# Kernel optimization log

Hardware: AMD Instinct MI355X
Metric: run time of the kernel (lower is better)

Reference implementation:

```python
import jax, jax.numpy as jnp
import numpy as np

N_NODES = 20000
N_EDGES = 320000
NUM_GRAPHS = 64
IN_DIM = 256


def setup_inputs() -> dict:
    key = jax.random.key(0)
    ks = jax.random.split(key, 12)
    x = jax.random.normal(ks[0], (N_NODES, IN_DIM), dtype=jnp.float32)
    edge_index = jax.random.randint(ks[1], (2, N_EDGES), 0, N_NODES, dtype=jnp.int64)
    batch = jnp.sort(jax.random.randint(ks[2], (N_NODES,), 0, NUM_GRAPHS, dtype=jnp.int64))
    def glorot(k, shape):
        lim = float(np.sqrt(6.0 / (shape[0] + shape[1])))
        return jax.random.uniform(k, shape, dtype=jnp.float32, minval=-lim, maxval=lim)
    W1 = glorot(ks[3], (IN_DIM, 256)); b1 = jnp.zeros((256,), jnp.float32)
    W2 = glorot(ks[4], (256, 128));   b2 = jnp.zeros((128,), jnp.float32)
    Wl1 = glorot(ks[5], (128, 64));   bl1 = jnp.zeros((64,), jnp.float32)
    Wl2 = glorot(ks[6], (64, 1));     bl2 = jnp.zeros((1,), jnp.float32)
    return {"x": x, "edge_index": edge_index, "batch": batch,
            "W1": W1, "b1": b1, "W2": W2, "b2": b2,
            "Wl1": Wl1, "bl1": bl1, "Wl2": Wl2, "bl2": bl2}


def gcn_conv(x, src, dst, W, b, n_nodes):
    # PyG GCNConv: add self-loops, symmetric normalization D^-1/2 (A+I) D^-1/2,
    # linear transform first, then gather-scale-scatter aggregation, then bias.
    loop = jnp.arange(n_nodes, dtype=src.dtype)
    s = jnp.concatenate([src, loop])
    d = jnp.concatenate([dst, loop])
    deg = jax.ops.segment_sum(jnp.ones_like(d, dtype=x.dtype), d, num_segments=n_nodes)
    dinv = jnp.where(deg > 0, jax.lax.rsqrt(deg), 0.0)
    norm = dinv[s] * dinv[d]                         # [E+N]
    h = x @ W                                        # [N, out]
    msg = h[s] * norm[:, None]                       # [E+N, out]
    out = jax.ops.segment_sum(msg, d, num_segments=n_nodes)
    return out + b


def global_mean_pool(x, batch, num_graphs):
    sums = jax.ops.segment_sum(x, batch, num_segments=num_graphs)
    cnts = jax.ops.segment_sum(jnp.ones((x.shape[0],), x.dtype), batch, num_segments=num_graphs)
    return sums / jnp.maximum(cnts, 1.0)[:, None]


def reference(x, edge_index, batch, W1, b1, W2, b2, Wl1, bl1, Wl2, bl2):
    n = x.shape[0]
    src, dst = edge_index[0], edge_index[1]
    h = jax.nn.relu(gcn_conv(x, src, dst, W1, b1, n))   # dropout = identity (eval)
    h = jax.nn.relu(gcn_conv(h, src, dst, W2, b2, n))
    g = global_mean_pool(h, batch, NUM_GRAPHS)          # [G, 128]
    g = jax.nn.relu(g @ Wl1 + bl1)
    return jax.nn.sigmoid(g @ Wl2 + bl2)                # [G, 1]
```

## Files before the change

kernel.cpp:

```cpp
#include <hip/hip_runtime.h>
#include <hip/hip_bf16.h>
#include <math.h>

typedef __attribute__((ext_vector_type(8))) short bf16x8;
typedef __attribute__((ext_vector_type(4))) float f32x4;

__device__ __forceinline__ unsigned short f2bf(float f) {
    unsigned int u = __float_as_uint(f);
    unsigned int r = (u + 0x7FFFu + ((u >> 16) & 1u)) >> 16;
    return (unsigned short)r;
}
__device__ __forceinline__ float bf2f(unsigned short h) {
    return __uint_as_float(((unsigned int)h) << 16);
}
__device__ __forceinline__ float bfe(short s) {
    return __uint_as_float(((unsigned int)(unsigned short)s) << 16);
}
__device__ __forceinline__ unsigned char f2fp8(float v) {
    int p = __builtin_amdgcn_cvt_pk_fp8_f32(v, v, 0, false);
    return (unsigned char)(p & 0xff);
}
__device__ __forceinline__ unsigned int pk4fp8(float a, float b, float c, float d) {
    int p = __builtin_amdgcn_cvt_pk_fp8_f32(a, b, 0, false);
    p = __builtin_amdgcn_cvt_pk_fp8_f32(c, d, p, true);
    return (unsigned int)p;
}
__device__ __forceinline__ void fp8x8_fma(uint2 u, float w, float* a) {
    a[0] += __builtin_amdgcn_cvt_f32_fp8((int)u.x, 0) * w;
    a[1] += __builtin_amdgcn_cvt_f32_fp8((int)u.x, 1) * w;
    a[2] += __builtin_amdgcn_cvt_f32_fp8((int)u.x, 2) * w;
    a[3] += __builtin_amdgcn_cvt_f32_fp8((int)u.x, 3) * w;
    a[4] += __builtin_amdgcn_cvt_f32_fp8((int)u.y, 0) * w;
    a[5] += __builtin_amdgcn_cvt_f32_fp8((int)u.y, 1) * w;
    a[6] += __builtin_amdgcn_cvt_f32_fp8((int)u.y, 2) * w;
    a[7] += __builtin_amdgcn_cvt_f32_fp8((int)u.y, 3) * w;
}
__device__ __forceinline__ void fp8x4_fma(unsigned int u, float w, float* a) {
    a[0] += __builtin_amdgcn_cvt_f32_fp8((int)u, 0) * w;
    a[1] += __builtin_amdgcn_cvt_f32_fp8((int)u, 1) * w;
    a[2] += __builtin_amdgcn_cvt_f32_fp8((int)u, 2) * w;
    a[3] += __builtin_amdgcn_cvt_f32_fp8((int)u, 3) * w;
}
__device__ __forceinline__ float deg_dinv(int c) { return rsqrtf((float)c + 1.0f); }

__device__ __forceinline__ void load_lds16(const unsigned short* g, unsigned short* l) {
    __builtin_amdgcn_global_load_lds(
        (const __attribute__((address_space(1))) unsigned int*)g,
        (__attribute__((address_space(3))) unsigned int*)l, 16, 0, 0);
}

__global__ __launch_bounds__(256) void prep_kernel(const int* __restrict__ src,
                                                   const int* __restrict__ dst,
                                                   int* __restrict__ cnt,
                                                   int* __restrict__ csr,
                                                   const float* __restrict__ x,
                                                   unsigned short* __restrict__ xh,
                                                   const int* __restrict__ batch,
                                                   int* __restrict__ gstart,
                                                   const float* __restrict__ W1,
                                                   unsigned short* __restrict__ w1th,
                                                   unsigned short* __restrict__ w1tl,
                                                   const float* __restrict__ W2,
                                                   unsigned short* __restrict__ w2th,
                                                   unsigned short* __restrict__ w2tl,
                                                   int N, int E, int G,
                                                   int FB, int CXB, int BNB) {
    int b = blockIdx.x;
    int tid = threadIdx.x;
    if (b < FB) {
        int e = b * 256 + tid;
        if (e < E) {
            int d = dst[e];
            int slot = atomicAdd(&cnt[d], 1);
            if (slot < 64) csr[(d << 6) + slot] = src[e];
        }
        return;
    }
    b -= FB;
    if (b < CXB) {
        size_t idx = (size_t)b * 256 + tid;
        size_t total4 = (size_t)N * 64;
        if (idx < total4) {
            float4 v = ((const float4*)x)[idx];
            ushort4 o;
            o.x = f2bf(v.x); o.y = f2bf(v.y); o.z = f2bf(v.z); o.w = f2bf(v.w);
            ((ushort4*)xh)[idx] = o;
        }
        return;
    }
    b -= CXB;
    if (b < BNB) {
        int i = b * 256 + tid;
        if (i >= N) return;
        int bb = batch[i];
        if (i == 0) { for (int g = 0; g <= bb; g++) gstart[g] = 0; }
        else { int bp = batch[i - 1]; for (int g = bp + 1; g <= bb; g++) gstart[g] = i; }
        if (i == N - 1) { for (int g = bb + 1; g <= G; g++) gstart[g] = N; }
        return;
    }
    b -= BNB;
    {
        int idx = b * 256 + tid;
        if (idx < 256 * 256) {
            int m = idx >> 8, k = idx & 255;
            float w = W1[(size_t)k * 256 + m];
            unsigned short hi = f2bf(w);
            w1th[idx] = hi;
            w1tl[idx] = f2bf(w - bf2f(hi));
        } else if (idx < 256 * 256 + 128 * 256) {
            int j = idx - 256 * 256;
            int m = j >> 8, k = j & 255;
            float w = W2[(size_t)k * 128 + m];
            unsigned short hi = f2bf(w);
            w2th[j] = hi;
            w2tl[j] = f2bf(w - bf2f(hi));
        }
    }
}

__global__ __launch_bounds__(256) void gemm_kernel(const unsigned short* __restrict__ A,
                                                   const unsigned short* __restrict__ Bth,
                                                   const unsigned short* __restrict__ Btl,
                                                   unsigned char* __restrict__ C8,
                                                   int N, int M) {
    __shared__ unsigned short As[128 * 32];
    __shared__ unsigned short Bhs[64 * 32];
    __shared__ unsigned short Bls[64 * 32];
    const int K = 256;
    int tid = threadIdx.x;
    int wave = tid >> 6, lane = tid & 63;
    int quad = lane >> 4, m16 = lane & 15;
    int r0 = blockIdx.y * 128, c0 = blockIdx.x * 64;
    int srow = lane >> 2;
    int skoff = (lane & 3) * 8;

    f32x4 acc[2][4];
#pragma unroll
    for (int rg = 0; rg < 2; rg++)
#pragma unroll
        for (int ct = 0; ct < 4; ct++) acc[rg][ct] = (f32x4){0.f, 0.f, 0.f, 0.f};

    for (int kb = 0; kb < K; kb += 32) {
#pragma unroll
        for (int i = 0; i < 2; i++) {
            int brow = wave * 32 + i * 16 + srow;
            int grow = r0 + brow; if (grow >= N) grow = N - 1;
            load_lds16(A + (size_t)grow * K + kb + skoff, As + (wave * 32 + i * 16) * 32);
        }
        {
            int bcol = wave * 16 + srow;
            size_t goff = (size_t)(c0 + bcol) * K + kb + skoff;
            load_lds16(Bth + goff, Bhs + (wave * 16) * 32);
            load_lds16(Btl + goff, Bls + (wave * 16) * 32);
        }
        __syncthreads();
        bf16x8 af[2], bh[4], bl[4];
#pragma unroll
        for (int rg = 0; rg < 2; rg++)
            af[rg] = *(const bf16x8*)(As + (wave * 32 + rg * 16 + m16) * 32 + quad * 8);
#pragma unroll
        for (int ct = 0; ct < 4; ct++) {
            bh[ct] = *(const bf16x8*)(Bhs + (ct * 16 + m16) * 32 + quad * 8);
            bl[ct] = *(const bf16x8*)(Bls + (ct * 16 + m16) * 32 + quad * 8);
        }
#pragma unroll
        for (int rg = 0; rg < 2; rg++)
#pragma unroll
            for (int ct = 0; ct < 4; ct++) {
                acc[rg][ct] = __builtin_amdgcn_mfma_f32_16x16x32_bf16(af[rg], bh[ct], acc[rg][ct], 0, 0, 0);
                acc[rg][ct] = __builtin_amdgcn_mfma_f32_16x16x32_bf16(af[rg], bl[ct], acc[rg][ct], 0, 0, 0);
            }
        __syncthreads();
    }
#pragma unroll
    for (int rg = 0; rg < 2; rg++) {
#pragma unroll
        for (int ct = 0; ct < 4; ct++) {
            int col = c0 + ct * 16 + m16;
#pragma unroll
            for (int r = 0; r < 4; r++) {
                int row = r0 + wave * 32 + rg * 16 + quad * 4 + r;
                if (row < N) C8[(size_t)row * M + col] = f2fp8(acc[rg][ct][r]);
            }
        }
    }
}

__global__ __launch_bounds__(256) void gather256_kernel(const unsigned char* __restrict__ h8,
                                                        const int* __restrict__ csr,
                                                        const int* __restrict__ cnt,
                                                        const float* __restrict__ bias,
                                                        unsigned short* __restrict__ out, int N) {
    int node = blockIdx.x * 4 + (threadIdx.x >> 6);
    if (node >= N) return;
    int lane = threadIdx.x & 63;
    int half = lane >> 5, hl = lane & 31;
    int beg = node << 6;
    int c = cnt[node]; if (c > 64) c = 64;
    int end = beg + c;
    float a[8] = {0, 0, 0, 0, 0, 0, 0, 0};
    int j = beg;
    for (; j + 7 < end; j += 8) {
        int s0 = csr[j + half], s1 = csr[j + 2 + half];
        int s2 = csr[j + 4 + half], s3 = csr[j + 6 + half];
        float w0 = deg_dinv(cnt[s0]), w1 = deg_dinv(cnt[s1]);
        float w2 = deg_dinv(cnt[s2]), w3 = deg_dinv(cnt[s3]);
        uint2 u0 = *(const uint2*)(h8 + (size_t)s0 * 256 + hl * 8);
        uint2 u1 = *(const uint2*)(h8 + (size_t)s1 * 256 + hl * 8);
        uint2 u2 = *(const uint2*)(h8 + (size_t)s2 * 256 + hl * 8);
        uint2 u3 = *(const uint2*)(h8 + (size_t)s3 * 256 + hl * 8);
        fp8x8_fma(u0, w0, a); fp8x8_fma(u1, w1, a);
        fp8x8_fma(u2, w2, a); fp8x8_fma(u3, w3, a);
    }
    for (; j + 1 < end; j += 2) {
        int s0 = csr[j + half];
        float w0 = deg_dinv(cnt[s0]);
        uint2 u0 = *(const uint2*)(h8 + (size_t)s0 * 256 + hl * 8);
        fp8x8_fma(u0, w0, a);
    }
    if (j < end && half == 0) {
        int s0 = csr[j];
        float w0 = deg_dinv(cnt[s0]);
        uint2 u0 = *(const uint2*)(h8 + (size_t)s0 * 256 + hl * 8);
        fp8x8_fma(u0, w0, a);
    }
#pragma unroll
    for (int i = 0; i < 8; i++) a[i] += __shfl_down(a[i], 32);
    if (half == 0) {
        float dd = deg_dinv(c);
        float self[8] = {0, 0, 0, 0, 0, 0, 0, 0};
        uint2 uh = *(const uint2*)(h8 + (size_t)node * 256 + hl * 8);
        fp8x8_fma(uh, dd, self);
        float4 bv0 = ((const float4*)bias)[hl * 2];
        float4 bv1 = ((const float4*)bias)[hl * 2 + 1];
        float bvf[8] = {bv0.x, bv0.y, bv0.z, bv0.w, bv1.x, bv1.y, bv1.z, bv1.w};
        bf16x8 o;
#pragma unroll
        for (int i = 0; i < 8; i++)
            o[i] = (short)f2bf(fmaxf((a[i] + self[i]) * dd + bvf[i], 0.f));
        ((bf16x8*)(out + (size_t)node * 256))[hl] = o;
    }
}

__global__ __launch_bounds__(256) void gather128_kernel(const unsigned char* __restrict__ t8,
                                                        const int* __restrict__ csr,
                                                        const int* __restrict__ cnt,
                                                        const float* __restrict__ bias,
                                                        unsigned char* __restrict__ out2, int N) {
    int node = blockIdx.x * 4 + (threadIdx.x >> 6);
    if (node >= N) return;
    int lane = threadIdx.x & 63;
    int half = lane >> 5, hl = lane & 31;
    int beg = node << 6;
    int c = cnt[node]; if (c > 64) c = 64;
    int end = beg + c;
    float a[4] = {0, 0, 0, 0};
    int j = beg;
    for (; j + 7 < end; j += 8) {
        int s0 = csr[j + half], s1 = csr[j + 2 + half];
        int s2 = csr[j + 4 + half], s3 = csr[j + 6 + half];
        float w0 = deg_dinv(cnt[s0]), w1 = deg_dinv(cnt[s1]);
        float w2 = deg_dinv(cnt[s2]), w3 = deg_dinv(cnt[s3]);
        unsigned int u0 = *(const unsigned int*)(t8 + (size_t)s0 * 128 + hl * 4);
        unsigned int u1 = *(const unsigned int*)(t8 + (size_t)s1 * 128 + hl * 4);
        unsigned int u2 = *(const unsigned int*)(t8 + (size_t)s2 * 128 + hl * 4);
        unsigned int u3 = *(const unsigned int*)(t8 + (size_t)s3 * 128 + hl * 4);
        fp8x4_fma(u0, w0, a); fp8x4_fma(u1, w1, a);
        fp8x4_fma(u2, w2, a); fp8x4_fma(u3, w3, a);
    }
    for (; j + 1 < end; j += 2) {
        int s0 = csr[j + half];
        float w0 = deg_dinv(cnt[s0]);
        unsigned int u0 = *(const unsigned int*)(t8 + (size_t)s0 * 128 + hl * 4);
        fp8x4_fma(u0, w0, a);
    }
    if (j < end && half == 0) {
        int s0 = csr[j];
        float w0 = deg_dinv(cnt[s0]);
        unsigned int u0 = *(const unsigned int*)(t8 + (size_t)s0 * 128 + hl * 4);
        fp8x4_fma(u0, w0, a);
    }
#pragma unroll
    for (int i = 0; i < 4; i++) a[i] += __shfl_down(a[i], 32);
    if (half == 0) {
        float dd = deg_dinv(c);
        float self[4] = {0, 0, 0, 0};
        unsigned int uh = *(const unsigned int*)(t8 + (size_t)node * 128 + hl * 4);
        fp8x4_fma(uh, dd, self);
        float4 bv = ((const float4*)bias)[hl];
        float r0 = fmaxf((a[0] + self[0]) * dd + bv.x, 0.f);
        float r1 = fmaxf((a[1] + self[1]) * dd + bv.y, 0.f);
        float r2 = fmaxf((a[2] + self[2]) * dd + bv.z, 0.f);
        float r3 = fmaxf((a[3] + self[3]) * dd + bv.w, 0.f);
        ((unsigned int*)(out2 + (size_t)node * 128))[hl] = pk4fp8(r0, r1, r2, r3);
    }
}

__global__ __launch_bounds__(256) void poolhead_kernel(const unsigned char* __restrict__ out2,
                                                       const int* __restrict__ gstart,
                                                       const float* __restrict__ Wl1,
                                                       const float* __restrict__ bl1,
                                                       const float* __restrict__ Wl2,
                                                       const float* __restrict__ bl2,
                                                       float* __restrict__ out) {
    int g = blockIdx.x;
    int tid = threadIdx.x;
    int hw = tid >> 5, hl = tid & 31;
    int gs = gstart[g], ge = gstart[g + 1];
    float a[4] = {0, 0, 0, 0};
    int i = gs + hw;
    for (; i + 8 < ge; i += 16) {
        unsigned int u0 = ((const unsigned int*)(out2 + (size_t)i * 128))[hl];
        unsigned int u1 = ((const unsigned int*)(out2 + (size_t)(i + 8) * 128))[hl];
        fp8x4_fma(u0, 1.0f, a);
        fp8x4_fma(u1, 1.0f, a);
    }
    if (i < ge) {
        unsigned int u0 = ((const unsigned int*)(out2 + (size_t)i * 128))[hl];
        fp8x4_fma(u0, 1.0f, a);
    }
    __shared__ float red[8][128];
#pragma unroll
    for (int k = 0; k < 4; k++) red[hw][hl * 4 + k] = a[k];
    __syncthreads();
    __shared__ float gv[128];
    if (tid < 128) {
        float s = 0.f;
#pragma unroll
        for (int w = 0; w < 8; w++) s += red[w][tid];
        float cntf = fmaxf((float)(ge - gs), 1.0f);
        gv[tid] = s / cntf;
    }
    __syncthreads();
    if (tid < 64) {
        float acc = bl1[tid];
#pragma unroll 8
        for (int k = 0; k < 128; k++) acc += gv[k] * Wl1[k * 64 + tid];
        acc = fmaxf(acc, 0.f);
        float p = acc * Wl2[tid];
#pragma unroll
        for (int off = 32; off; off >>= 1) p += __shfl_down(p, off);
        if (tid == 0) out[g] = 1.f / (1.f + expf(-(p + bl2[0])));
    }
}

extern "C" void kernel_launch(void* const* d_in, const int* in_sizes, int n_in,
                              void* d_out, int out_size, void* d_ws, size_t ws_size,
                              hipStream_t stream) {
    const float* x   = (const float*)d_in[0];
    const int* ei    = (const int*)d_in[1];
    const int* batch = (const int*)d_in[2];
    const float* W1  = (const float*)d_in[3];
    const float* b1  = (const float*)d_in[4];
    const float* W2  = (const float*)d_in[5];
    const float* b2  = (const float*)d_in[6];
    const float* Wl1 = (const float*)d_in[7];
    const float* bl1 = (const float*)d_in[8];
    const float* Wl2 = (const float*)d_in[9];
    const float* bl2 = (const float*)d_in[10];
    float* out = (float*)d_out;

    const int N = in_sizes[2];
    const int E = in_sizes[1] / 2;
    const int G = 64;
    const int* src = ei;
    const int* dst = ei + E;

    char* base = (char*)d_ws;
    size_t off = 0;
    auto carve = [&](size_t bytes) -> char* {
        char* p = base + off;
        off = (off + bytes + 15) & ~(size_t)15;
        return p;
    };
    int*   cnt    = (int*)carve((size_t)N * 4);
    int*   csr    = (int*)carve((size_t)N * 64 * 4);
    int*   gstart = (int*)carve((size_t)(G + 1) * 4);
    unsigned short* w1th = (unsigned short*)carve((size_t)256 * 256 * 2);
    unsigned short* w1tl = (unsigned short*)carve((size_t)256 * 256 * 2);
    unsigned short* w2th = (unsigned short*)carve((size_t)128 * 256 * 2);
    unsigned short* w2tl = (unsigned short*)carve((size_t)128 * 256 * 2);
    unsigned short* xh   = (unsigned short*)carve((size_t)N * 256 * 2);
    unsigned char*  h8   = (unsigned char*)carve((size_t)N * 256);
    unsigned short* o1h  = (unsigned short*)carve((size_t)N * 256 * 2);
    unsigned char* t8   = (unsigned char*)xh;
    unsigned char* out2 = h8;

    hipMemsetAsync(cnt, 0, (size_t)N * 4, stream);

    const int FB  = (E + 255) / 256;
    const int CXB = (int)(((size_t)N * 64 + 255) / 256);
    const int BNB = (N + 255) / 256;
    const int CWB = (256 * 256 + 128 * 256 + 255) / 256;
    prep_kernel<<<FB + CXB + BNB + CWB, 256, 0, stream>>>(
        src, dst, cnt, csr, x, xh, batch, gstart, W1, w1th, w1tl, W2, w2th, w2tl,
        N, E, G, FB, CXB, BNB);

    {
        dim3 grid(4, (N + 127) / 128);
        gemm_kernel<<<grid, 256, 0, stream>>>(xh, w1th, w1tl, h8, N, 256);
    }
    gather256_kernel<<<(N + 3) / 4, 256, 0, stream>>>(h8, csr, cnt, b1, o1h, N);

    {
        dim3 grid(2, (N + 127) / 128);
        gemm_kernel<<<grid, 256, 0, stream>>>(o1h, w2th, w2tl, t8, N, 128);
    }
    gather128_kernel<<<(N + 3) / 4, 256, 0, stream>>>(t8, csr, cnt, b2, out2, N);

    poolhead_kernel<<<G, 256, 0, stream>>>(out2, gstart, Wl1, bl1, Wl2, bl2, out);
}
```

Baseline: 175.4 us.

## Fuse all stages into one cooperative persistent kernel with grid syncs

Replaces the memset plus six separate kernel launches with a single cooperative persistent kernel. Stages are separated by grid-wide barriers, and each stage's work is distributed over a grid-stride loop. The CSR edge fill now runs concurrently with the first GEMM tiles, since the GEMM does not depend on it. The aim is to remove launch overhead and inter-kernel gaps, at the cost of grid.sync latency and a persistent grid sized from occupancy (capped at 2048 blocks), which may lower per-stage parallelism.

```diff
diff --git a/kernel.cpp b/kernel.cpp
--- a/kernel.cpp
+++ b/kernel.cpp
@@ -1,6 +1,9 @@
 #include <hip/hip_runtime.h>
 #include <hip/hip_bf16.h>
+#include <hip/hip_cooperative_groups.h>
 #include <math.h>
+
+namespace cg = cooperative_groups;
 
 typedef __attribute__((ext_vector_type(8))) short bf16x8;
 typedef __attribute__((ext_vector_type(4))) float f32x4;
@@ -12,9 +15,6 @@
 }
 __device__ __forceinline__ float bf2f(unsigned short h) {
     return __uint_as_float(((unsigned int)h) << 16);
-}
-__device__ __forceinline__ float bfe(short s) {
-    return __uint_as_float(((unsigned int)(unsigned short)s) << 16);
 }
 __device__ __forceinline__ unsigned char f2fp8(float v) {
     int p = __builtin_amdgcn_cvt_pk_fp8_f32(v, v, 0, false);
@@ -49,7 +49,74 @@
         (__attribute__((address_space(3))) unsigned int*)l, 16, 0, 0);
 }
 
-__global__ __launch_bounds__(256) void prep_kernel(const int* __restrict__ src,
+__device__ __forceinline__ void gemm_tile_body(const unsigned short* __restrict__ A,
+                                               const unsigned short* __restrict__ Bth,
+                                               const unsigned short* __restrict__ Btl,
+                                               unsigned char* __restrict__ C8,
+                                               int N, int M, int bx, int by,
+                                               unsigned short* As, unsigned short* Bhs,
+                                               unsigned short* Bls) {
+    const int K = 256;
+    int tid = threadIdx.x;
+    int wave = tid >> 6, lane = tid & 63;
+    int quad = lane >> 4, m16 = lane & 15;
+    int r0 = by * 128, c0 = bx * 64;
+    int srow = lane >> 2;
+    int skoff = (lane & 3) * 8;
+
+    f32x4 acc[2][4];
+#pragma unroll
+    for (int rg = 0; rg < 2; rg++)
+#pragma unroll
+        for (int ct = 0; ct < 4; ct++) acc[rg][ct] = (f32x4){0.f, 0.f, 0.f, 0.f};
+
+    for (int kb = 0; kb < K; kb += 32) {
+#pragma unroll
+        for (int i = 0; i < 2; i++) {
+            int brow = wave * 32 + i * 16 + srow;
+            int grow = r0 + brow; if (grow >= N) grow = N - 1;
+            load_lds16(A + (size_t)grow * K + kb + skoff, As + (wave * 32 + i * 16) * 32);
+        }
+        {
+            int bcol = wave * 16 + srow;
+            size_t goff = (size_t)(c0 + bcol) * K + kb + skoff;
+            load_lds16(Bth + goff, Bhs + (wave * 16) * 32);
+            load_lds16(Btl + goff, Bls + (wave * 16) * 32);
+        }
+        __syncthreads();
+        bf16x8 af[2], bh[4], bl[4];
+#pragma unroll
+        for (int rg = 0; rg < 2; rg++)
+            af[rg] = *(const bf16x8*)(As + (wave * 32 + rg * 16 + m16) * 32 + quad * 8);
+#pragma unroll
+        for (int ct = 0; ct < 4; ct++) {
+            bh[ct] = *(const bf16x8*)(Bhs + (ct * 16 + m16) * 32 + quad * 8);
+            bl[ct] = *(const bf16x8*)(Bls + (ct * 16 + m16) * 32 + quad * 8);
+        }
+#pragma unroll
+        for (int rg = 0; rg < 2; rg++)
+#pragma unroll
+            for (int ct = 0; ct < 4; ct++) {
+                acc[rg][ct] = __builtin_amdgcn_mfma_f32_16x16x32_bf16(af[rg], bh[ct], acc[rg][ct], 0, 0, 0);
+                acc[rg][ct] = __builtin_amdgcn_mfma_f32_16x16x32_bf16(af[rg], bl[ct], acc[rg][ct], 0, 0, 0);
+            }
+        __syncthreads();
+    }
+#pragma unroll
+    for (int rg = 0; rg < 2; rg++) {
+#pragma unroll
+        for (int ct = 0; ct < 4; ct++) {
+            int col = c0 + ct * 16 + m16;
+#pragma unroll
+            for (int r = 0; r < 4; r++) {
+                int row = r0 + wave * 32 + rg * 16 + quad * 4 + r;
+                if (row < N) C8[(size_t)row * M + col] = f2fp8(acc[rg][ct][r]);
+            }
+        }
+    }
+}
+
+__global__ __launch_bounds__(256) void mega_kernel(const int* __restrict__ src,
                                                    const int* __restrict__ dst,
                                                    int* __restrict__ cnt,
                                                    int* __restrict__ csr,
@@ -63,284 +130,256 @@
                                                    const float* __restrict__ W2,
                                                    unsigned short* __restrict__ w2th,
                                                    unsigned short* __restrict__ w2tl,
-                                                   int N, int E, int G,
-                                                   int FB, int CXB, int BNB) {
-    int b = blockIdx.x;
+                                                   const float* __restrict__ b1,
+                                                   unsigned char* __restrict__ h8,
+                                                   unsigned short* __restrict__ o1h,
+                                                   const float* __restrict__ b2,
+                                                   unsigned char* __restrict__ t8,
+                                                   unsigned char* __restrict__ out2,
+                                                   const float* __restrict__ Wl1,
+                                                   const float* __restrict__ bl1,
+                                                   const float* __restrict__ Wl2,
+                                                   const float* __restrict__ bl2,
+                                                   float* __restrict__ out,
+                                                   int N, int E, int G) {
+    __shared__ unsigned short smem[128 * 32 + 64 * 32 + 64 * 32];
+    unsigned short* As  = smem;
+    unsigned short* Bhs = smem + 128 * 32;
+    unsigned short* Bls = smem + 128 * 32 + 64 * 32;
+    cg::grid_group grid = cg::this_grid();
     int tid = threadIdx.x;
-    if (b < FB) {
-        int e = b * 256 + tid;
-        if (e < E) {
-            int d = dst[e];
-            int slot = atomicAdd(&cnt[d], 1);
-            if (slot < 64) csr[(d << 6) + slot] = src[e];
-        }
-        return;
-    }
-    b -= FB;
-    if (b < CXB) {
-        size_t idx = (size_t)b * 256 + tid;
-        size_t total4 = (size_t)N * 64;
-        if (idx < total4) {
-            float4 v = ((const float4*)x)[idx];
-            ushort4 o;
-            o.x = f2bf(v.x); o.y = f2bf(v.y); o.z = f2bf(v.z); o.w = f2bf(v.w);
-            ((ushort4*)xh)[idx] = o;
-        }
-        return;
-    }
-    b -= CXB;
-    if (b < BNB) {
-        int i = b * 256 + tid;
-        if (i >= N) return;
-        int bb = batch[i];
-        if (i == 0) { for (int g = 0; g <= bb; g++) gstart[g] = 0; }
-        else { int bp = batch[i - 1]; for (int g = bp + 1; g <= bb; g++) gstart[g] = i; }
-        if (i == N - 1) { for (int g = bb + 1; g <= G; g++) gstart[g] = N; }
-        return;
-    }
-    b -= BNB;
+    int nblk = gridDim.x;
+
     {
-        int idx = b * 256 + tid;
-        if (idx < 256 * 256) {
-            int m = idx >> 8, k = idx & 255;
-            float w = W1[(size_t)k * 256 + m];
-            unsigned short hi = f2bf(w);
-            w1th[idx] = hi;
-            w1tl[idx] = f2bf(w - bf2f(hi));
-        } else if (idx < 256 * 256 + 128 * 256) {
-            int j = idx - 256 * 256;
-            int m = j >> 8, k = j & 255;
-            float w = W2[(size_t)k * 128 + m];
-            unsigned short hi = f2bf(w);
-            w2th[j] = hi;
-            w2tl[j] = f2bf(w - bf2f(hi));
-        }
-    }
-}
-
-__global__ __launch_bounds__(256) void gemm_kernel(const unsigned short* __restrict__ A,
-                                                   const unsigned short* __restrict__ Bth,
-                                                   const unsigned short* __restrict__ Btl,
-                                                   unsigned char* __restrict__ C8,
-                                                   int N, int M) {
-    __shared__ unsigned short As[128 * 32];
-    __shared__ unsigned short Bhs[64 * 32];
-    __shared__ unsigned short Bls[64 * 32];
-    const int K = 256;
-    int tid = threadIdx.x;
-    int wave = tid >> 6, lane = tid & 63;
-    int quad = lane >> 4, m16 = lane & 15;
-    int r0 = blockIdx.y * 128, c0 = blockIdx.x * 64;
-    int srow = lane >> 2;
-    int skoff = (lane & 3) * 8;
-
-    f32x4 acc[2][4];
-#pragma unroll
-    for (int rg = 0; rg < 2; rg++)
-#pragma unroll
-        for (int ct = 0; ct < 4; ct++) acc[rg][ct] = (f32x4){0.f, 0.f, 0.f, 0.f};
-
-    for (int kb = 0; kb < K; kb += 32) {
-#pragma unroll
-        for (int i = 0; i < 2; i++) {
-            int brow = wave * 32 + i * 16 + srow;
-            int grow = r0 + brow; if (grow >= N) grow = N - 1;
-            load_lds16(A + (size_t)grow * K + kb + skoff, As + (wave * 32 + i * 16) * 32);
-        }
-        {
-            int bcol = wave * 16 + srow;
-            size_t goff = (size_t)(c0 + bcol) * K + kb + skoff;
-            load_lds16(Bth + goff, Bhs + (wave * 16) * 32);
-            load_lds16(Btl + goff, Bls + (wave * 16) * 32);
-        }
+        const int ZB  = (N + 255) >> 8;
+        const int CXB = (int)(((size_t)N * 64 + 255) >> 8);
+        const int BNB = (N + 255) >> 8;
+        const int CWB = (256 * 256 + 128 * 256 + 255) >> 8;
+        const int TOT = ZB + CXB + BNB + CWB;
+        for (int b = blockIdx.x; b < TOT; b += nblk) {
+            int bb = b;
+            if (bb < ZB) {
+                int i = bb * 256 + tid;
+                if (i < N) cnt[i] = 0;
+                continue;
+            }
+            bb -= ZB;
+            if (bb < CXB) {
+                size_t idx = (size_t)bb * 256 + tid;
+                if (idx < (size_t)N * 64) {
+                    float4 v = ((const float4*)x)[idx];
+                    ushort4 o;
+                    o.x = f2bf(v.x); o.y = f2bf(v.y); o.z = f2bf(v.z); o.w = f2bf(v.w);
+                    ((ushort4*)xh)[idx] = o;
+                }
+                continue;
+            }
+            bb -= CXB;
+            if (bb < BNB) {
+                int i = bb * 256 + tid;
+                if (i < N) {
+                    int bv = batch[i];
+                    if (i == 0) { for (int g = 0; g <= bv; g++) gstart[g] = 0; }
+                    else { int bp = batch[i - 1]; for (int g = bp + 1; g <= bv; g++) gstart[g] = i; }
+                    if (i == N - 1) { for (int g = bv + 1; g <= G; g++) gstart[g] = N; }
+                }
+                continue;
+            }
+            bb -= BNB;
+            {
+                int idx = bb * 256 + tid;
+                if (idx < 256 * 256) {
+                    int m = idx >> 8, k = idx & 255;
+                    float w = W1[(size_t)k * 256 + m];
+                    unsigned short hi = f2bf(w);
+                    w1th[idx] = hi;
+                    w1tl[idx] = f2bf(w - bf2f(hi));
+                } else if (idx < 256 * 256 + 128 * 256) {
+                    int j = idx - 256 * 256;
+                    int m = j >> 8, k = j & 255;
+                    float w = W2[(size_t)k * 128 + m];
+                    unsigned short hi = f2bf(w);
+                    w2th[j] = hi;
+                    w2tl[j] = f2bf(w - bf2f(hi));
+                }
+            }
+        }
+    }
+    grid.sync();
+
+    {
+        const int FB = (E + 255) >> 8;
+        const int T1 = (N + 127) >> 7;
+        const int TOT = FB + 4 * T1;
+        for (int b = blockIdx.x; b < TOT; b += nblk) {
+            if (b < FB) {
+                int e = b * 256 + tid;
+                if (e < E) {
+                    int d = dst[e];
+                    int slot = atomicAdd(&cnt[d], 1);
+                    if (slot < 64) csr[(d << 6) + slot] = src[e];
+                }
+            } else {
+                int gb = b - FB;
+                gemm_tile_body(xh, w1th, w1tl, h8, N, 256, gb & 3, gb >> 2, As, Bhs, Bls);
+            }
+        }
+    }
+    grid.sync();
+
+    for (int base = blockIdx.x * 4; base < N; base += nblk * 4) {
+        int node = base + (tid >> 6);
+        if (node < N) {
+            int lane = tid & 63;
+            int half = lane >> 5, hl = lane & 31;
+            int beg = node << 6;
+            int c = cnt[node]; if (c > 64) c = 64;
+            int end = beg + c;
+            float a[8] = {0, 0, 0, 0, 0, 0, 0, 0};
+            int j = beg;
+            for (; j + 7 < end; j += 8) {
+                int s0 = csr[j + half], s1 = csr[j + 2 + half];
+                int s2 = csr[j + 4 + half], s3 = csr[j + 6 + half];
+                float w0 = deg_dinv(cnt[s0]), w1 = deg_dinv(cnt[s1]);
+                float w2 = deg_dinv(cnt[s2]), w3 = deg_dinv(cnt[s3]);
+                uint2 u0 = *(const uint2*)(h8 + (size_t)s0 * 256 + hl * 8);
+                uint2 u1 = *(const uint2*)(h8 + (size_t)s1 * 256 + hl * 8);
+                uint2 u2 = *(const uint2*)(h8 + (size_t)s2 * 256 + hl * 8);
+                uint2 u3 = *(const uint2*)(h8 + (size_t)s3 * 256 + hl * 8);
+                fp8x8_fma(u0, w0, a); fp8x8_fma(u1, w1, a);
+                fp8x8_fma(u2, w2, a); fp8x8_fma(u3, w3, a);
+            }
+            for (; j + 1 < end; j += 2) {
+                int s0 = csr[j + half];
+                float w0 = deg_dinv(cnt[s0]);
+                uint2 u0 = *(const uint2*)(h8 + (size_t)s0 * 256 + hl * 8);
+                fp8x8_fma(u0, w0, a);
+            }
+            if (j < end && half == 0) {
+                int s0 = csr[j];
+                float w0 = deg_dinv(cnt[s0]);
+                uint2 u0 = *(const uint2*)(h8 + (size_t)s0 * 256 + hl * 8);
+                fp8x8_fma(u0, w0, a);
+            }
+#pragma unroll
+            for (int i = 0; i < 8; i++) a[i] += __shfl_down(a[i], 32);
+            if (half == 0) {
+                float dd = deg_dinv(c);
+                float self[8] = {0, 0, 0, 0, 0, 0, 0, 0};
+                uint2 uh = *(const uint2*)(h8 + (size_t)node * 256 + hl * 8);
+                fp8x8_fma(uh, dd, self);
+                float4 bv0 = ((const float4*)b1)[hl * 2];
+                float4 bv1 = ((const float4*)b1)[hl * 2 + 1];
+                float bvf[8] = {bv0.x, bv0.y, bv0.z, bv0.w, bv1.x, bv1.y, bv1.z, bv1.w};
+                bf16x8 o;
+#pragma unroll
+                for (int i = 0; i < 8; i++)
+                    o[i] = (short)f2bf(fmaxf((a[i] + self[i]) * dd + bvf[i], 0.f));
+                ((bf16x8*)(o1h + (size_t)node * 256))[hl] = o;
+            }
+        }
+    }
+    grid.sync();
+
+    {
+        const int T1 = (N + 127) >> 7;
+        for (int b = blockIdx.x; b < 2 * T1; b += nblk)
+            gemm_tile_body(o1h, w2th, w2tl, t8, N, 128, b & 1, b >> 1, As, Bhs, Bls);
+    }
+    grid.sync();
+
+    for (int base = blockIdx.x * 4; base < N; base += nblk * 4) {
+        int node = base + (tid >> 6);
+        if (node < N) {
+            int lane = tid & 63;
+            int half = lane >> 5, hl = lane & 31;
+            int beg = node << 6;
+            int c = cnt[node]; if (c > 64) c = 64;
+            int end = beg + c;
+            float a[4] = {0, 0, 0, 0};
+            int j = beg;
+            for (; j + 7 < end; j += 8) {
+                int s0 = csr[j + half], s1 = csr[j + 2 + half];
+                int s2 = csr[j + 4 + half], s3 = csr[j + 6 + half];
+                float w0 = deg_dinv(cnt[s0]), w1 = deg_dinv(cnt[s1]);
+                float w2 = deg_dinv(cnt[s2]), w3 = deg_dinv(cnt[s3]);
+                unsigned int u0 = *(const unsigned int*)(t8 + (size_t)s0 * 128 + hl * 4);
+                unsigned int u1 = *(const unsigned int*)(t8 + (size_t)s1 * 128 + hl * 4);
+                unsigned int u2 = *(const unsigned int*)(t8 + (size_t)s2 * 128 + hl * 4);
+                unsigned int u3 = *(const unsigned int*)(t8 + (size_t)s3 * 128 + hl * 4);
+                fp8x4_fma(u0, w0, a); fp8x4_fma(u1, w1, a);
+                fp8x4_fma(u2, w2, a); fp8x4_fma(u3, w3, a);
+            }
+            for (; j + 1 < end; j += 2) {
+                int s0 = csr[j + half];
+                float w0 = deg_dinv(cnt[s0]);
+                unsigned int u0 = *(const unsigned int*)(t8 + (size_t)s0 * 128 + hl * 4);
+                fp8x4_fma(u0, w0, a);
+            }
+            if (j < end && half == 0) {
+                int s0 = csr[j];
+                float w0 = deg_dinv(cnt[s0]);
+                unsigned int u0 = *(const unsigned int*)(t8 + (size_t)s0 * 128 + hl * 4);
+                fp8x4_fma(u0, w0, a);
+            }
+#pragma unroll
+            for (int i = 0; i < 4; i++) a[i] += __shfl_down(a[i], 32);
+            if (half == 0) {
+                float dd = deg_dinv(c);
+                float self[4] = {0, 0, 0, 0};
+                unsigned int uh = *(const unsigned int*)(t8 + (size_t)node * 128 + hl * 4);
+                fp8x4_fma(uh, dd, self);
+                float4 bv = ((const float4*)b2)[hl];
+                float r0 = fmaxf((a[0] + self[0]) * dd + bv.x, 0.f);
+                float r1 = fmaxf((a[1] + self[1]) * dd + bv.y, 0.f);
+                float r2 = fmaxf((a[2] + self[2]) * dd + bv.z, 0.f);
+                float r3 = fmaxf((a[3] + self[3]) * dd + bv.w, 0.f);
+                ((unsigned int*)(out2 + (size_t)node * 128))[hl] = pk4fp8(r0, r1, r2, r3);
+            }
+        }
+    }
+    grid.sync();
+
+    if (blockIdx.x < (unsigned)G) {
+        int g = blockIdx.x;
+        int hw = tid >> 5, hl = tid & 31;
+        int gs = gstart[g], ge = gstart[g + 1];
+        float a[4] = {0, 0, 0, 0};
+        int i = gs + hw;
+        for (; i + 8 < ge; i += 16) {
+            unsigned int u0 = ((const unsigned int*)(out2 + (size_t)i * 128))[hl];
+            unsigned int u1 = ((const unsigned int*)(out2 + (size_t)(i + 8) * 128))[hl];
+            fp8x4_fma(u0, 1.0f, a);
+            fp8x4_fma(u1, 1.0f, a);
+        }
+        if (i < ge) {
+            unsigned int u0 = ((const unsigned int*)(out2 + (size_t)i * 128))[hl];
+            fp8x4_fma(u0, 1.0f, a);
+        }
+        float* red = (float*)smem;
+        float* gv  = red + 8 * 128;
         __syncthreads();
-        bf16x8 af[2], bh[4], bl[4];
-#pragma unroll
-        for (int rg = 0; rg < 2; rg++)
-            af[rg] = *(const bf16x8*)(As + (wave * 32 + rg * 16 + m16) * 32 + quad * 8);
-#pragma unroll
-        for (int ct = 0; ct < 4; ct++) {
-            bh[ct] = *(const bf16x8*)(Bhs + (ct * 16 + m16) * 32 + quad * 8);
-            bl[ct] = *(const bf16x8*)(Bls + (ct * 16 + m16) * 32 + quad * 8);
-        }
-#pragma unroll
-        for (int rg = 0; rg < 2; rg++)
-#pragma unroll
-            for (int ct = 0; ct < 4; ct++) {
-                acc[rg][ct] = __builtin_amdgcn_mfma_f32_16x16x32_bf16(af[rg], bh[ct], acc[rg][ct], 0, 0, 0);
-                acc[rg][ct] = __builtin_amdgcn_mfma_f32_16x16x32_bf16(af[rg], bl[ct], acc[rg][ct], 0, 0, 0);
-            }
+#pragma unroll
+        for (int k = 0; k < 4; k++) red[hw * 128 + hl * 4 + k] = a[k];
         __syncthreads();
-    }
-#pragma unroll
-    for (int rg = 0; rg < 2; rg++) {
-#pragma unroll
-        for (int ct = 0; ct < 4; ct++) {
-            int col = c0 + ct * 16 + m16;
-#pragma unroll
-            for (int r = 0; r < 4; r++) {
-                int row = r0 + wave * 32 + rg * 16 + quad * 4 + r;
-                if (row < N) C8[(size_t)row * M + col] = f2fp8(acc[rg][ct][r]);
-            }
-        }
-    }
-}
-
-__global__ __launch_bounds__(256) void gather256_kernel(const unsigned char* __restrict__ h8,
-                                                        const int* __restrict__ csr,
-                                                        const int* __restrict__ cnt,
-                                                        const float* __restrict__ bias,
-                                                        unsigned short* __restrict__ out, int N) {
-    int node = blockIdx.x * 4 + (threadIdx.x >> 6);
-    if (node >= N) return;
-    int lane = threadIdx.x & 63;
-    int half = lane >> 5, hl = lane & 31;
-    int beg = node << 6;
-    int c = cnt[node]; if (c > 64) c = 64;
-    int end = beg + c;
-    float a[8] = {0, 0, 0, 0, 0, 0, 0, 0};
-    int j = beg;
-    for (; j + 7 < end; j += 8) {
-        int s0 = csr[j + half], s1 = csr[j + 2 + half];
-        int s2 = csr[j + 4 + half], s3 = csr[j + 6 + half];
-        float w0 = deg_dinv(cnt[s0]), w1 = deg_dinv(cnt[s1]);
-        float w2 = deg_dinv(cnt[s2]), w3 = deg_dinv(cnt[s3]);
-        uint2 u0 = *(const uint2*)(h8 + (size_t)s0 * 256 + hl * 8);
-        uint2 u1 = *(const uint2*)(h8 + (size_t)s1 * 256 + hl * 8);
-        uint2 u2 = *(const uint2*)(h8 + (size_t)s2 * 256 + hl * 8);
-        uint2 u3 = *(const uint2*)(h8 + (size_t)s3 * 256 + hl * 8);
-        fp8x8_fma(u0, w0, a); fp8x8_fma(u1, w1, a);
-        fp8x8_fma(u2, w2, a); fp8x8_fma(u3, w3, a);
-    }
-    for (; j + 1 < end; j += 2) {
-        int s0 = csr[j + half];
-        float w0 = deg_dinv(cnt[s0]);
-        uint2 u0 = *(const uint2*)(h8 + (size_t)s0 * 256 + hl * 8);
-        fp8x8_fma(u0, w0, a);
-    }
-    if (j < end && half == 0) {
-        int s0 = csr[j];
-        float w0 = deg_dinv(cnt[s0]);
-        uint2 u0 = *(const uint2*)(h8 + (size_t)s0 * 256 + hl * 8);
-        fp8x8_fma(u0, w0, a);
-    }
-#pragma unroll
-    for (int i = 0; i < 8; i++) a[i] += __shfl_down(a[i], 32);
-    if (half == 0) {
-        float dd = deg_dinv(c);
-        float self[8] = {0, 0, 0, 0, 0, 0, 0, 0};
-        uint2 uh = *(const uint2*)(h8 + (size_t)node * 256 + hl * 8);
-        fp8x8_fma(uh, dd, self);
-        float4 bv0 = ((const float4*)bias)[hl * 2];
-        float4 bv1 = ((const float4*)bias)[hl * 2 + 1];
-        float bvf[8] = {bv0.x, bv0.y, bv0.z, bv0.w, bv1.x, bv1.y, bv1.z, bv1.w};
-        bf16x8 o;
-#pragma unroll
-        for (int i = 0; i < 8; i++)
-            o[i] = (short)f2bf(fmaxf((a[i] + self[i]) * dd + bvf[i], 0.f));
-        ((bf16x8*)(out + (size_t)node * 256))[hl] = o;
-    }
-}
-
-__global__ __launch_bounds__(256) void gather128_kernel(const unsigned char* __restrict__ t8,
-                                                        const int* __restrict__ csr,
-                                                        const int* __restrict__ cnt,
-                                                        const float* __restrict__ bias,
-                                                        unsigned char* __restrict__ out2, int N) {
-    int node = blockIdx.x * 4 + (threadIdx.x >> 6);
-    if (node >= N) return;
-    int lane = threadIdx.x & 63;
-    int half = lane >> 5, hl = lane & 31;
-    int beg = node << 6;
-    int c = cnt[node]; if (c > 64) c = 64;
-    int end = beg + c;
-    float a[4] = {0, 0, 0, 0};
-    int j = beg;
-    for (; j + 7 < end; j += 8) {
-        int s0 = csr[j + half], s1 = csr[j + 2 + half];
-        int s2 = csr[j + 4 + half], s3 = csr[j + 6 + half];
-        float w0 = deg_dinv(cnt[s0]), w1 = deg_dinv(cnt[s1]);
-        float w2 = deg_dinv(cnt[s2]), w3 = deg_dinv(cnt[s3]);
-        unsigned int u0 = *(const unsigned int*)(t8 + (size_t)s0 * 128 + hl * 4);
-        unsigned int u1 = *(const unsigned int*)(t8 + (size_t)s1 * 128 + hl * 4);
-        unsigned int u2 = *(const unsigned int*)(t8 + (size_t)s2 * 128 + hl * 4);
-        unsigned int u3 = *(const unsigned int*)(t8 + (size_t)s3 * 128 + hl * 4);
-        fp8x4_fma(u0, w0, a); fp8x4_fma(u1, w1, a);
-        fp8x4_fma(u2, w2, a); fp8x4_fma(u3, w3, a);
-    }
-    for (; j + 1 < end; j += 2) {
-        int s0 = csr[j + half];
-        float w0 = deg_dinv(cnt[s0]);
-        unsigned int u0 = *(const unsigned int*)(t8 + (size_t)s0 * 128 + hl * 4);
-        fp8x4_fma(u0, w0, a);
-    }
-    if (j < end && half == 0) {
-        int s0 = csr[j];
-        float w0 = deg_dinv(cnt[s0]);
-        unsigned int u0 = *(const unsigned int*)(t8 + (size_t)s0 * 128 + hl * 4);
-        fp8x4_fma(u0, w0, a);
-    }
-#pragma unroll
-    for (int i = 0; i < 4; i++) a[i] += __shfl_down(a[i], 32);
-    if (half == 0) {
-        float dd = deg_dinv(c);
-        float self[4] = {0, 0, 0, 0};
-        unsigned int uh = *(const unsigned int*)(t8 + (size_t)node * 128 + hl * 4);
-        fp8x4_fma(uh, dd, self);
-        float4 bv = ((const float4*)bias)[hl];
-        float r0 = fmaxf((a[0] + self[0]) * dd + bv.x, 0.f);
-        float r1 = fmaxf((a[1] + self[1]) * dd + bv.y, 0.f);
-        float r2 = fmaxf((a[2] + self[2]) * dd + bv.z, 0.f);
-        float r3 = fmaxf((a[3] + self[3]) * dd + bv.w, 0.f);
-        ((unsigned int*)(out2 + (size_t)node * 128))[hl] = pk4fp8(r0, r1, r2, r3);
-    }
-}
-
-__global__ __launch_bounds__(256) void poolhead_kernel(const unsigned char* __restrict__ out2,
-                                                       const int* __restrict__ gstart,
-                                                       const float* __restrict__ Wl1,
-                                                       const float* __restrict__ bl1,
-                                                       const float* __restrict__ Wl2,
-                                                       const float* __restrict__ bl2,
-                                                       float* __restrict__ out) {
-    int g = blockIdx.x;
-    int tid = threadIdx.x;
-    int hw = tid >> 5, hl = tid & 31;
-    int gs = gstart[g], ge = gstart[g + 1];
-    float a[4] = {0, 0, 0, 0};
-    int i = gs + hw;
-    for (; i + 8 < ge; i += 16) {
-        unsigned int u0 = ((const unsigned int*)(out2 + (size_t)i * 128))[hl];
-        unsigned int u1 = ((const unsigned int*)(out2 + (size_t)(i + 8) * 128))[hl];
-        fp8x4_fma(u0, 1.0f, a);
-        fp8x4_fma(u1, 1.0f, a);
-    }
-    if (i < ge) {
-        unsigned int u0 = ((const unsigned int*)(out2 + (size_t)i * 128))[hl];
-        fp8x4_fma(u0, 1.0f, a);
-    }
-    __shared__ float red[8][128];
-#pragma unroll
-    for (int k = 0; k < 4; k++) red[hw][hl * 4 + k] = a[k];
-    __syncthreads();
-    __shared__ float gv[128];
-    if (tid < 128) {
-        float s = 0.f;
-#pragma unroll
-        for (int w = 0; w < 8; w++) s += red[w][tid];
-        float cntf = fmaxf((float)(ge - gs), 1.0f);
-        gv[tid] = s / cntf;
-    }
-    __syncthreads();
-    if (tid < 64) {
-        float acc = bl1[tid];
+        if (tid < 128) {
+            float s = 0.f;
+#pragma unroll
+            for (int w = 0; w < 8; w++) s += red[w * 128 + tid];
+            float cntf = fmaxf((float)(ge - gs), 1.0f);
+            gv[tid] = s / cntf;
+        }
+        __syncthreads();
+        if (tid < 64) {
+            float acc = bl1[tid];
 #pragma unroll 8
-        for (int k = 0; k < 128; k++) acc += gv[k] * Wl1[k * 64 + tid];
-        acc = fmaxf(acc, 0.f);
-        float p = acc * Wl2[tid];
-#pragma unroll
-        for (int off = 32; off; off >>= 1) p += __shfl_down(p, off);
-        if (tid == 0) out[g] = 1.f / (1.f + expf(-(p + bl2[0])));
+            for (int k = 0; k < 128; k++) acc += gv[k] * Wl1[k * 64 + tid];
+            acc = fmaxf(acc, 0.f);
+            float p = acc * Wl2[tid];
+#pragma unroll
+            for (int off = 32; off; off >>= 1) p += __shfl_down(p, off);
+            if (tid == 0) out[g] = 1.f / (1.f + expf(-(p + bl2[0])));
+        }
     }
 }
 
@@ -360,9 +399,9 @@
     const float* bl2 = (const float*)d_in[10];
     float* out = (float*)d_out;
 
-    const int N = in_sizes[2];
-    const int E = in_sizes[1] / 2;
-    const int G = 64;
+    int N = in_sizes[2];
+    int E = in_sizes[1] / 2;
+    int G = 64;
     const int* src = ei;
     const int* dst = ei + E;
 
@@ -386,27 +425,18 @@
     unsigned char* t8   = (unsigned char*)xh;
     unsigned char* out2 = h8;
 
-    hipMemsetAsync(cnt, 0, (size_t)N * 4, stream);
-
-    const int FB  = (E + 255) / 256;
-    const int CXB = (int)(((size_t)N * 64 + 255) / 256);
-    const int BNB = (N + 255) / 256;
-    const int CWB = (256 * 256 + 128 * 256 + 255) / 256;
-    prep_kernel<<<FB + CXB + BNB + CWB, 256, 0, stream>>>(
-        src, dst, cnt, csr, x, xh, batch, gstart, W1, w1th, w1tl, W2, w2th, w2tl,
-        N, E, G, FB, CXB, BNB);
-
-    {
-        dim3 grid(4, (N + 127) / 128);
-        gemm_kernel<<<grid, 256, 0, stream>>>(xh, w1th, w1tl, h8, N, 256);
-    }
-    gather256_kernel<<<(N + 3) / 4, 256, 0, stream>>>(h8, csr, cnt, b1, o1h, N);
-
-    {
-        dim3 grid(2, (N + 127) / 128);
-        gemm_kernel<<<grid, 256, 0, stream>>>(o1h, w2th, w2tl, t8, N, 128);
-    }
-    gather128_kernel<<<(N + 3) / 4, 256, 0, stream>>>(t8, csr, cnt, b2, out2, N);
-
-    poolhead_kernel<<<G, 256, 0, stream>>>(out2, gstart, Wl1, bl1, Wl2, bl2, out);
-}
+    int nb = 0;
+    hipOccupancyMaxActiveBlocksPerMultiprocessor(&nb, mega_kernel, 256, 0);
+    if (nb < 1) nb = 1;
+    int grid = nb * 256;
+    if (grid > 2048) grid = 2048;
+
+    void* args[] = {
+        (void*)&src, (void*)&dst, (void*)&cnt, (void*)&csr, (void*)&x, (void*)&xh,
+        (void*)&batch, (void*)&gstart, (void*)&W1, (void*)&w1th, (void*)&w1tl,
+        (void*)&W2, (void*)&w2th, (void*)&w2tl, (void*)&b1, (void*)&h8, (void*)&o1h,
+        (void*)&b2, (void*)&t8, (void*)&out2, (void*)&Wl1, (void*)&bl1,
+        (void*)&Wl2, (void*)&bl2, (void*)&out, (void*)&N, (void*)&E, (void*)&G
+    };
+    hipLaunchCooperativeKernel((void*)mega_kernel, dim3(grid), dim3(256), args, 0, stream);
+}
```

Result: slower. 521.4 us (+197.2%).
